# Kernel tuning notes

Measured on AMD Instinct MI355X. Metric: run time of the kernel, lower is better.

Reference implementation:

```python
import jax, jax.numpy as jnp
import numpy as np

HIDDEN = 100

def _lstm_step(h, c, gx, Whh, bhh):
    # gx: precomputed input contribution W_ih @ x + b_ih, shape [4H]
    gates = gx + Whh @ h + bhh
    i, f, g, o = jnp.split(gates, 4)
    i = jax.nn.sigmoid(i)
    f = jax.nn.sigmoid(f)
    g = jnp.tanh(g)
    o = jax.nn.sigmoid(o)
    c = f * c + i * g
    h = o * jnp.tanh(c)
    return h, c


def setup_inputs() -> dict:
    key = jax.random.key(0)
    ks = jax.random.split(key, 12)
    s = 0.1
    T_enc, T_dec = 4096, 4096
    return {
        "x": jax.random.normal(ks[0], (1, T_enc, 3), jnp.float32),
        "y": jax.random.randint(ks[1], (1, T_dec), 0, 6),
        "enc_Wih": jax.random.normal(ks[2], (4 * HIDDEN, 3), jnp.float32) * s,
        "enc_Whh": jax.random.normal(ks[3], (4 * HIDDEN, HIDDEN), jnp.float32) * s,
        "enc_bih": jax.random.normal(ks[4], (4 * HIDDEN,), jnp.float32) * s,
        "enc_bhh": jax.random.normal(ks[5], (4 * HIDDEN,), jnp.float32) * s,
        "dec_Wih": jax.random.normal(ks[6], (4 * HIDDEN, 1), jnp.float32) * s,
        "dec_Whh": jax.random.normal(ks[7], (4 * HIDDEN, HIDDEN), jnp.float32) * s,
        "dec_bih": jax.random.normal(ks[8], (4 * HIDDEN,), jnp.float32) * s,
        "dec_bhh": jax.random.normal(ks[9], (4 * HIDDEN,), jnp.float32) * s,
        "lin_W": jax.random.normal(ks[10], (6, HIDDEN), jnp.float32) * s,
        "lin_b": jax.random.normal(ks[11], (6,), jnp.float32) * s,
        "teacher_forcing_ratio": 1,
        "n_classes": 6,
    }


def reference(x, y, enc_Wih, enc_Whh, enc_bih, enc_bhh,
              dec_Wih, dec_Whh, dec_bih, dec_bhh, lin_W, lin_b,
              teacher_forcing_ratio, n_classes):
    T_dec = y.shape[1]
    # ---- Encoder: batch=1 LSTM over source sequence ----
    gx_enc = x[0] @ enc_Wih.T + enc_bih  # [T_enc, 4H]

    def enc_step(carry, gx):
        h, c = carry
        h, c = _lstm_step(h, c, gx, enc_Whh, enc_bhh)
        return (h, c), None

    h0 = jnp.zeros((HIDDEN,), x.dtype)
    (h_enc, c_enc), _ = jax.lax.scan(enc_step, (h0, h0), gx_enc)

    # ---- Decoder: single-step loop with teacher forcing ----
    yf = y[0].astype(jnp.float32)          # target labels fed as floats
    ratio = jnp.float32(teacher_forcing_ratio)
    u = jax.random.uniform(jax.random.key(1), (T_dec - 1,), jnp.float32)

    def dec_step(carry, inp):
        h, c, dec_in = carry
        u_t, y_t = inp
        gx = dec_in * dec_Wih[:, 0] + dec_bih  # scalar input -> [4H]
        h, c = _lstm_step(h, c, gx, dec_Whh, dec_bhh)
        logits = lin_W @ h + lin_b             # [n_classes]
        top_pred = jnp.argmax(logits).astype(jnp.float32)
        new_in = jnp.where(u_t < ratio, y_t, top_pred)
        return (h, c, new_in), logits

    _, logits_seq = jax.lax.scan(dec_step, (h_enc, c_enc, yf[0]), (u, yf[1:]))
    # outputs[0][t-1] = logits at step t, t = 1..T_dec-1; last row stays zero
    outputs = jnp.zeros((1, T_dec, n_classes), jnp.float32)
    outputs = outputs.at[0, : T_dec - 1].set(logits_seq)
    return outputs
```

## Files before the change

### kernel.cpp

```cpp
#include <hip/hip_runtime.h>

typedef _Float16 h2_t __attribute__((ext_vector_type(2)));

#define HID  100
#define TENC 4096
#define TDEC 4096
#define NCLS 6
#define NTHR 256

__device__ __forceinline__ float sigm(float v)  { return __builtin_amdgcn_rcpf(1.0f + __expf(-v)); }
__device__ __forceinline__ float tanh_(float v) { return 1.0f - 2.0f * __builtin_amdgcn_rcpf(1.0f + __expf(2.0f * v)); }

#define SYNC_LDS() asm volatile("s_waitcnt lgkmcnt(0)\n\ts_barrier" ::: "memory")

__device__ __forceinline__ float packh2(float a, float b) {
    h2_t p; p[0] = (_Float16)a; p[1] = (_Float16)b;
    return __builtin_bit_cast(float, p);
}

__device__ __forceinline__ float xsum1(float v) {
    const int s = __builtin_amdgcn_update_dpp(
        0, __builtin_bit_cast(int, v), 0xB1, 0xF, 0xF, true);
    return v + __builtin_bit_cast(float, s);
}

__device__ __forceinline__ float fd2(float w, float h, float acc) {
    return __builtin_amdgcn_fdot2(__builtin_bit_cast(h2_t, w),
                                  __builtin_bit_cast(h2_t, h), acc, false);
}

__global__ __launch_bounds__(NTHR, 1)
void lstm_rec(const float* __restrict__ x,
              const int*   __restrict__ y,
              const float* __restrict__ eWih,
              const float* __restrict__ eWhh,
              const float* __restrict__ ebih,
              const float* __restrict__ ebhh,
              const float* __restrict__ dWih,
              const float* __restrict__ dWhh,
              const float* __restrict__ dbih,
              const float* __restrict__ dbhh,
              float* __restrict__ hsto)
{
    __shared__ __align__(16) _Float16 hbuf[2][2][80];
    __shared__ __align__(8)  uint2    xst[TENC];
    __shared__               unsigned yst[TDEC];

    const int  t     = threadIdx.x;
    const int  w     = t >> 6;
    const int  l     = t & 63;
    const int  khalf = l & 1;
    const int  cell  = w * 32 + (l >> 1);
    const bool live  = (cell < HID);
    const int  k0    = khalf * 50;

    for (int i = t; i < TENC; i += NTHR) {
        const float a = x[3*i], b = x[3*i+1], cc = x[3*i+2];
        uint2 u;
        u.x = __builtin_bit_cast(unsigned, packh2(a, b));
        u.y = __builtin_bit_cast(unsigned, packh2(cc, 1.0f));
        xst[i] = u;
    }
    for (int i = t; i < TDEC; i += NTHR)
        yst[i] = __builtin_bit_cast(unsigned, packh2((float)y[i], 0.0f));
    for (int i = t; i < 2*2*80; i += NTHR) ((_Float16*)hbuf)[i] = (_Float16)0.0f;

    float wf[4][25];
    float wxp[4][2], bs[4];
    float c = 0.0f;
    #pragma unroll
    for (int r = 0; r < 4; ++r) {
        #pragma unroll
        for (int j = 0; j < 25; ++j) wf[r][j] = 0.0f;
        wxp[r][0] = wxp[r][1] = 0.0f; bs[r] = 0.0f;
    }
    if (live) {
        #pragma unroll
        for (int r = 0; r < 4; ++r) {
            const int row = cell + r * HID;
            #pragma unroll
            for (int j = 0; j < 25; ++j)
                wf[r][j] = packh2(eWhh[row*HID + k0 + 2*j], eWhh[row*HID + k0 + 2*j + 1]);
            if (khalf == 0) {
                wxp[r][0] = packh2(eWih[row*3+0], eWih[row*3+1]);
                wxp[r][1] = packh2(eWih[row*3+2], 0.0f);
                bs[r]     = ebih[row] + ebhh[row];
            }
        }
    }
    __syncthreads();

    const int hh2  = (cell < 50) ? 0 : 1;
    const int hoff = cell - 50 * hh2;

    int p = 0;

    for (int s = 0; s < TENC; ++s) {
        const float4* h4 = (const float4*)&hbuf[p][khalf][0];
        float hp[25];
        #pragma unroll
        for (int j = 0; j < 6; ++j) {
            const float4 v = h4[j];
            hp[4*j+0] = v.x; hp[4*j+1] = v.y; hp[4*j+2] = v.z; hp[4*j+3] = v.w;
        }
        hp[24] = ((const float*)h4)[24];

        const uint2 xp = xst[s];
        const float x0 = __builtin_bit_cast(float, xp.x);
        const float x1 = __builtin_bit_cast(float, xp.y);
        float a0 = fd2(wxp[0][0], x0, fd2(wxp[0][1], x1, bs[0]));
        float a1 = fd2(wxp[1][0], x0, fd2(wxp[1][1], x1, bs[1]));
        float a2 = fd2(wxp[2][0], x0, fd2(wxp[2][1], x1, bs[2]));
        float a3 = fd2(wxp[3][0], x0, fd2(wxp[3][1], x1, bs[3]));
        float b0 = 0.0f, b1 = 0.0f, b2 = 0.0f, b3 = 0.0f;
        #pragma unroll
        for (int j = 0; j < 12; ++j) {
            a0 = fd2(wf[0][j], hp[j], a0);
            a1 = fd2(wf[1][j], hp[j], a1);
            a2 = fd2(wf[2][j], hp[j], a2);
            a3 = fd2(wf[3][j], hp[j], a3);
        }
        #pragma unroll
        for (int j = 12; j < 25; ++j) {
            b0 = fd2(wf[0][j], hp[j], b0);
            b1 = fd2(wf[1][j], hp[j], b1);
            b2 = fd2(wf[2][j], hp[j], b2);
            b3 = fd2(wf[3][j], hp[j], b3);
        }
        a0 += b0; a1 += b1; a2 += b2; a3 += b3;

        a0 = xsum1(a0);
        a1 = xsum1(a1);
        a2 = xsum1(a2);
        a3 = xsum1(a3);

        const float fi = sigm(a0), ff = sigm(a1), fg = tanh_(a2), fo = sigm(a3);
        c = ff * c + fi * fg;
        const float hn = fo * tanh_(c);
        if (khalf == 0 && live)
            hbuf[p ^ 1][hh2][hoff] = (_Float16)hn;
        SYNC_LDS();
        p ^= 1;
    }

    float wdp[4], bsd[4];
    #pragma unroll
    for (int r = 0; r < 4; ++r) { wdp[r] = 0.0f; bsd[r] = 0.0f; }
    if (live) {
        #pragma unroll
        for (int r = 0; r < 4; ++r) {
            const int row = cell + r * HID;
            #pragma unroll
            for (int j = 0; j < 25; ++j)
                wf[r][j] = packh2(dWhh[row*HID + k0 + 2*j], dWhh[row*HID + k0 + 2*j + 1]);
            if (khalf == 0) {
                wdp[r] = packh2(dWih[row], 0.0f);
                bsd[r] = dbih[row] + dbhh[row];
            }
        }
    }

    for (int s = 0; s < TDEC - 1; ++s) {
        const float4* h4 = (const float4*)&hbuf[p][khalf][0];
        float hp[25];
        #pragma unroll
        for (int j = 0; j < 6; ++j) {
            const float4 v = h4[j];
            hp[4*j+0] = v.x; hp[4*j+1] = v.y; hp[4*j+2] = v.z; hp[4*j+3] = v.w;
        }
        hp[24] = ((const float*)h4)[24];

        const float yp = __builtin_bit_cast(float, yst[s]);
        float a0 = fd2(wdp[0], yp, bsd[0]);
        float a1 = fd2(wdp[1], yp, bsd[1]);
        float a2 = fd2(wdp[2], yp, bsd[2]);
        float a3 = fd2(wdp[3], yp, bsd[3]);
        float b0 = 0.0f, b1 = 0.0f, b2 = 0.0f, b3 = 0.0f;
        #pragma unroll
        for (int j = 0; j < 12; ++j) {
            a0 = fd2(wf[0][j], hp[j], a0);
            a1 = fd2(wf[1][j], hp[j], a1);
            a2 = fd2(wf[2][j], hp[j], a2);
            a3 = fd2(wf[3][j], hp[j], a3);
        }
        #pragma unroll
        for (int j = 12; j < 25; ++j) {
            b0 = fd2(wf[0][j], hp[j], b0);
            b1 = fd2(wf[1][j], hp[j], b1);
            b2 = fd2(wf[2][j], hp[j], b2);
            b3 = fd2(wf[3][j], hp[j], b3);
        }
        a0 += b0; a1 += b1; a2 += b2; a3 += b3;

        a0 = xsum1(a0);
        a1 = xsum1(a1);
        a2 = xsum1(a2);
        a3 = xsum1(a3);

        const float fi = sigm(a0), ff = sigm(a1), fg = tanh_(a2), fo = sigm(a3);
        c = ff * c + fi * fg;
        const float hn = fo * tanh_(c);
        if (live) {
            if (khalf == 0) {
                hbuf[p ^ 1][hh2][hoff] = (_Float16)hn;
            } else {
                hsto[s * HID + cell] = hn;
            }
        }
        SYNC_LDS();
        p ^= 1;
    }
}

__global__ __launch_bounds__(256)
void logits_k(const float* __restrict__ hsto, const float* __restrict__ linW,
              const float* __restrict__ linb, float* __restrict__ out)
{
    const int idx = blockIdx.x * 256 + threadIdx.x;
    if (idx >= TDEC * NCLS) return;
    const int tt = idx / NCLS;
    const int r  = idx % NCLS;
    if (tt >= TDEC - 1) { out[idx] = 0.0f; return; }
    const float* h  = hsto + tt * HID;
    const float* wr = linW + r * HID;
    float a = linb[r];
    #pragma unroll 4
    for (int k = 0; k < HID; ++k) a += wr[k] * h[k];
    out[idx] = a;
}

extern "C" void kernel_launch(void* const* d_in, const int* in_sizes, int n_in,
                              void* d_out, int out_size, void* d_ws, size_t ws_size,
                              hipStream_t stream)
{
    const float* x    = (const float*)d_in[0];
    const int*   y    = (const int*)  d_in[1];
    const float* eWih = (const float*)d_in[2];
    const float* eWhh = (const float*)d_in[3];
    const float* ebih = (const float*)d_in[4];
    const float* ebhh = (const float*)d_in[5];
    const float* dWih = (const float*)d_in[6];
    const float* dWhh = (const float*)d_in[7];
    const float* dbih = (const float*)d_in[8];
    const float* dbhh = (const float*)d_in[9];
    const float* linW = (const float*)d_in[10];
    const float* linb = (const float*)d_in[11];
    float* out  = (float*)d_out;
    float* hsto = (float*)d_ws;

    lstm_rec<<<dim3(1), dim3(NTHR), 0, stream>>>(
        x, y, eWih, eWhh, ebih, ebhh, dWih, dWhh, dbih, dbhh, hsto);

    const int nout = TDEC * NCLS;
    logits_k<<<dim3((nout + 255) / 256), dim3(256), 0, stream>>>(hsto, linW, linb, out);
}
```

Before: 3.589 ms.

## Fold input and bias into recurrent dot product and split gate activations across lane pair

Folds the input projection and bias into the recurrent fp16 dot-product by appending x (or y) and a constant 1 to the shared hidden buffer. The K split becomes 52/52 with 26 packed weight pairs per gate, which removes the separate input fdot2 chain. Each lane of a pair now computes two of the four gate nonlinearities and swaps them with DPP, halving transcendental work per lane. The single accumulator chain per gate is longer than the earlier two-chain split, which may add dependency latency.

```diff
diff --git a/kernel.cpp b/kernel.cpp
--- a/kernel.cpp
+++ b/kernel.cpp
@@ -18,18 +18,18 @@
     return __builtin_bit_cast(float, p);
 }
 
-__device__ __forceinline__ float xsum1(float v) {
-    const int s = __builtin_amdgcn_update_dpp(
-        0, __builtin_bit_cast(int, v), 0xB1, 0xF, 0xF, true);
-    return v + __builtin_bit_cast(float, s);
-}
-
 __device__ __forceinline__ float fd2(float w, float h, float acc) {
     return __builtin_amdgcn_fdot2(__builtin_bit_cast(h2_t, w),
                                   __builtin_bit_cast(h2_t, h), acc, false);
 }
 
-__global__ __launch_bounds__(NTHR, 1)
+__device__ __forceinline__ float dppB1(float v) {
+    return __builtin_bit_cast(float, __builtin_amdgcn_update_dpp(
+        0, __builtin_bit_cast(int, v), 0xB1, 0xF, 0xF, true));
+}
+__device__ __forceinline__ float xsum1(float v) { return v + dppB1(v); }
+
+__global__ __launch_bounds__(NTHR, 1) __attribute__((amdgpu_waves_per_eu(1, 1)))
 void lstm_rec(const float* __restrict__ x,
               const int*   __restrict__ y,
               const float* __restrict__ eWih,
@@ -42,7 +42,7 @@
               const float* __restrict__ dbhh,
               float* __restrict__ hsto)
 {
-    __shared__ __align__(16) _Float16 hbuf[2][2][80];
+    __shared__ __align__(16) _Float16 hbuf2[2][2][56];
     __shared__ __align__(8)  uint2    xst[TENC];
     __shared__               unsigned yst[TDEC];
 
@@ -52,7 +52,10 @@
     const int  khalf = l & 1;
     const int  cell  = w * 32 + (l >> 1);
     const bool live  = (cell < HID);
-    const int  k0    = khalf * 50;
+
+    const float cs = (khalf == 0) ?  2.0f : -1.0f;
+    const float ms = (khalf == 0) ? -2.0f :  1.0f;
+    const float as = (khalf == 0) ?  1.0f :  0.0f;
 
     for (int i = t; i < TENC; i += NTHR) {
         const float a = x[3*i], b = x[3*i+1], cc = x[3*i+2];
@@ -63,146 +66,181 @@
     }
     for (int i = t; i < TDEC; i += NTHR)
         yst[i] = __builtin_bit_cast(unsigned, packh2((float)y[i], 0.0f));
-    for (int i = t; i < 2*2*80; i += NTHR) ((_Float16*)hbuf)[i] = (_Float16)0.0f;
-
-    float wf[4][25];
-    float wxp[4][2], bs[4];
-    float c = 0.0f;
+    if (t < 2*2*56) ((_Float16*)hbuf2)[t] = (_Float16)0.0f;
+    __syncthreads();
+
+    if (t == 0) {
+        uint2 u;
+        u.x = __builtin_bit_cast(unsigned, packh2(x[0], x[1]));
+        u.y = __builtin_bit_cast(unsigned, packh2(x[2], 1.0f));
+        *(uint2*)&hbuf2[0][1][48] = u;
+    }
+
+    float wf[4][26];
     #pragma unroll
     for (int r = 0; r < 4; ++r) {
-        #pragma unroll
-        for (int j = 0; j < 25; ++j) wf[r][j] = 0.0f;
-        wxp[r][0] = wxp[r][1] = 0.0f; bs[r] = 0.0f;
-    }
-    if (live) {
-        #pragma unroll
-        for (int r = 0; r < 4; ++r) {
-            const int row = cell + r * HID;
-            #pragma unroll
-            for (int j = 0; j < 25; ++j)
-                wf[r][j] = packh2(eWhh[row*HID + k0 + 2*j], eWhh[row*HID + k0 + 2*j + 1]);
-            if (khalf == 0) {
-                wxp[r][0] = packh2(eWih[row*3+0], eWih[row*3+1]);
-                wxp[r][1] = packh2(eWih[row*3+2], 0.0f);
-                bs[r]     = ebih[row] + ebhh[row];
+        const int row = r*HID + cell;
+        #pragma unroll
+        for (int j = 0; j < 26; ++j) {
+            const int k0 = 52*khalf + 2*j, k1 = k0 + 1;
+            float v0 = 0.0f, v1 = 0.0f;
+            if (live) {
+                v0 = (k0 < HID) ? eWhh[row*HID + k0]
+                   : (k0 < 103) ? eWih[row*3 + (k0 - 100)] : (ebih[row] + ebhh[row]);
+                v1 = (k1 < HID) ? eWhh[row*HID + k1]
+                   : (k1 < 103) ? eWih[row*3 + (k1 - 100)] : (ebih[row] + ebhh[row]);
             }
-        }
-    }
-    __syncthreads();
-
-    const int hh2  = (cell < 50) ? 0 : 1;
-    const int hoff = cell - 50 * hh2;
-
+            wf[r][j] = packh2(v0, v1);
+        }
+    }
+    SYNC_LDS();
+
+    const int hh2  = (cell < 52) ? 0 : 1;
+    const int hoff = cell - 52*hh2;
+
+    float c = 0.0f;
     int p = 0;
 
     for (int s = 0; s < TENC; ++s) {
-        const float4* h4 = (const float4*)&hbuf[p][khalf][0];
-        float hp[25];
-        #pragma unroll
-        for (int j = 0; j < 6; ++j) {
-            const float4 v = h4[j];
-            hp[4*j+0] = v.x; hp[4*j+1] = v.y; hp[4*j+2] = v.z; hp[4*j+3] = v.w;
-        }
-        hp[24] = ((const float*)h4)[24];
-
-        const uint2 xp = xst[s];
-        const float x0 = __builtin_bit_cast(float, xp.x);
-        const float x1 = __builtin_bit_cast(float, xp.y);
-        float a0 = fd2(wxp[0][0], x0, fd2(wxp[0][1], x1, bs[0]));
-        float a1 = fd2(wxp[1][0], x0, fd2(wxp[1][1], x1, bs[1]));
-        float a2 = fd2(wxp[2][0], x0, fd2(wxp[2][1], x1, bs[2]));
-        float a3 = fd2(wxp[3][0], x0, fd2(wxp[3][1], x1, bs[3]));
-        float b0 = 0.0f, b1 = 0.0f, b2 = 0.0f, b3 = 0.0f;
-        #pragma unroll
-        for (int j = 0; j < 12; ++j) {
+        const _Float16* hr = &hbuf2[p][khalf][0];
+        float hp[26];
+        {
+            const float4 g0 = *(const float4*)&hr[0];
+            const float4 g1 = *(const float4*)&hr[8];
+            const float4 g2 = *(const float4*)&hr[16];
+            const float4 g3 = *(const float4*)&hr[24];
+            const float4 g4 = *(const float4*)&hr[32];
+            const float4 g5 = *(const float4*)&hr[40];
+            const float2 g6 = *(const float2*)&hr[48];
+            hp[0]=g0.x; hp[1]=g0.y; hp[2]=g0.z; hp[3]=g0.w;
+            hp[4]=g1.x; hp[5]=g1.y; hp[6]=g1.z; hp[7]=g1.w;
+            hp[8]=g2.x; hp[9]=g2.y; hp[10]=g2.z; hp[11]=g2.w;
+            hp[12]=g3.x; hp[13]=g3.y; hp[14]=g3.z; hp[15]=g3.w;
+            hp[16]=g4.x; hp[17]=g4.y; hp[18]=g4.z; hp[19]=g4.w;
+            hp[20]=g5.x; hp[21]=g5.y; hp[22]=g5.z; hp[23]=g5.w;
+            hp[24]=g6.x; hp[25]=g6.y;
+        }
+
+        if (t == 0 && s + 1 < TENC)
+            *(uint2*)&hbuf2[p ^ 1][1][48] = xst[s + 1];
+
+        float a0 = 0.0f, a1 = 0.0f, a2 = 0.0f, a3 = 0.0f;
+        #pragma unroll
+        for (int j = 0; j < 26; ++j) {
             a0 = fd2(wf[0][j], hp[j], a0);
             a1 = fd2(wf[1][j], hp[j], a1);
             a2 = fd2(wf[2][j], hp[j], a2);
             a3 = fd2(wf[3][j], hp[j], a3);
         }
-        #pragma unroll
-        for (int j = 12; j < 25; ++j) {
-            b0 = fd2(wf[0][j], hp[j], b0);
-            b1 = fd2(wf[1][j], hp[j], b1);
-            b2 = fd2(wf[2][j], hp[j], b2);
-            b3 = fd2(wf[3][j], hp[j], b3);
-        }
-        a0 += b0; a1 += b1; a2 += b2; a3 += b3;
-
         a0 = xsum1(a0);
         a1 = xsum1(a1);
         a2 = xsum1(a2);
         a3 = xsum1(a3);
 
-        const float fi = sigm(a0), ff = sigm(a1), fg = tanh_(a2), fo = sigm(a3);
-        c = ff * c + fi * fg;
+        const float uA = khalf ? a1 : a0;
+        const float rA = sigm(uA);
+        const float uB = khalf ? a3 : a2;
+        const float eB = __expf(uB * cs);
+        const float rB = __builtin_fmaf(__builtin_amdgcn_rcpf(1.0f + eB), ms, as);
+        const float sA = dppB1(rA);
+        const float sB = dppB1(rB);
+        const float fi = khalf ? sA : rA;
+        const float ff = khalf ? rA : sA;
+        const float fg = khalf ? sB : rB;
+        const float fo = khalf ? rB : sB;
+
+        c = __builtin_fmaf(ff, c, fi * fg);
         const float hn = fo * tanh_(c);
         if (khalf == 0 && live)
-            hbuf[p ^ 1][hh2][hoff] = (_Float16)hn;
+            hbuf2[p ^ 1][hh2][hoff] = (_Float16)hn;
         SYNC_LDS();
         p ^= 1;
     }
 
-    float wdp[4], bsd[4];
+    if (t == 0) {
+        uint2 v;
+        v.x = (yst[0] & 0xFFFFu) | 0x3C000000u;
+        v.y = 0u;
+        *(uint2*)&hbuf2[p][1][48] = v;
+    }
+
     #pragma unroll
-    for (int r = 0; r < 4; ++r) { wdp[r] = 0.0f; bsd[r] = 0.0f; }
-    if (live) {
-        #pragma unroll
-        for (int r = 0; r < 4; ++r) {
-            const int row = cell + r * HID;
-            #pragma unroll
-            for (int j = 0; j < 25; ++j)
-                wf[r][j] = packh2(dWhh[row*HID + k0 + 2*j], dWhh[row*HID + k0 + 2*j + 1]);
-            if (khalf == 0) {
-                wdp[r] = packh2(dWih[row], 0.0f);
-                bsd[r] = dbih[row] + dbhh[row];
+    for (int r = 0; r < 4; ++r) {
+        const int row = r*HID + cell;
+        #pragma unroll
+        for (int j = 0; j < 26; ++j) {
+            const int k0 = 52*khalf + 2*j, k1 = k0 + 1;
+            float v0 = 0.0f, v1 = 0.0f;
+            if (live) {
+                v0 = (k0 < HID) ? dWhh[row*HID + k0]
+                   : (k0 == 100) ? dWih[row]
+                   : (k0 == 101) ? (dbih[row] + dbhh[row]) : 0.0f;
+                v1 = (k1 < HID) ? dWhh[row*HID + k1]
+                   : (k1 == 100) ? dWih[row]
+                   : (k1 == 101) ? (dbih[row] + dbhh[row]) : 0.0f;
             }
-        }
-    }
+            wf[r][j] = packh2(v0, v1);
+        }
+    }
+    SYNC_LDS();
 
     for (int s = 0; s < TDEC - 1; ++s) {
-        const float4* h4 = (const float4*)&hbuf[p][khalf][0];
-        float hp[25];
-        #pragma unroll
-        for (int j = 0; j < 6; ++j) {
-            const float4 v = h4[j];
-            hp[4*j+0] = v.x; hp[4*j+1] = v.y; hp[4*j+2] = v.z; hp[4*j+3] = v.w;
-        }
-        hp[24] = ((const float*)h4)[24];
-
-        const float yp = __builtin_bit_cast(float, yst[s]);
-        float a0 = fd2(wdp[0], yp, bsd[0]);
-        float a1 = fd2(wdp[1], yp, bsd[1]);
-        float a2 = fd2(wdp[2], yp, bsd[2]);
-        float a3 = fd2(wdp[3], yp, bsd[3]);
-        float b0 = 0.0f, b1 = 0.0f, b2 = 0.0f, b3 = 0.0f;
-        #pragma unroll
-        for (int j = 0; j < 12; ++j) {
+        const _Float16* hr = &hbuf2[p][khalf][0];
+        float hp[26];
+        {
+            const float4 g0 = *(const float4*)&hr[0];
+            const float4 g1 = *(const float4*)&hr[8];
+            const float4 g2 = *(const float4*)&hr[16];
+            const float4 g3 = *(const float4*)&hr[24];
+            const float4 g4 = *(const float4*)&hr[32];
+            const float4 g5 = *(const float4*)&hr[40];
+            const float2 g6 = *(const float2*)&hr[48];
+            hp[0]=g0.x; hp[1]=g0.y; hp[2]=g0.z; hp[3]=g0.w;
+            hp[4]=g1.x; hp[5]=g1.y; hp[6]=g1.z; hp[7]=g1.w;
+            hp[8]=g2.x; hp[9]=g2.y; hp[10]=g2.z; hp[11]=g2.w;
+            hp[12]=g3.x; hp[13]=g3.y; hp[14]=g3.z; hp[15]=g3.w;
+            hp[16]=g4.x; hp[17]=g4.y; hp[18]=g4.z; hp[19]=g4.w;
+            hp[20]=g5.x; hp[21]=g5.y; hp[22]=g5.z; hp[23]=g5.w;
+            hp[24]=g6.x; hp[25]=g6.y;
+        }
+
+        if (t == 0 && s + 1 < TDEC - 1) {
+            uint2 v;
+            v.x = (yst[s + 1] & 0xFFFFu) | 0x3C000000u;
+            v.y = 0u;
+            *(uint2*)&hbuf2[p ^ 1][1][48] = v;
+        }
+
+        float a0 = 0.0f, a1 = 0.0f, a2 = 0.0f, a3 = 0.0f;
+        #pragma unroll
+        for (int j = 0; j < 26; ++j) {
             a0 = fd2(wf[0][j], hp[j], a0);
             a1 = fd2(wf[1][j], hp[j], a1);
             a2 = fd2(wf[2][j], hp[j], a2);
             a3 = fd2(wf[3][j], hp[j], a3);
         }
-        #pragma unroll
-        for (int j = 12; j < 25; ++j) {
-            b0 = fd2(wf[0][j], hp[j], b0);
-            b1 = fd2(wf[1][j], hp[j], b1);
-            b2 = fd2(wf[2][j], hp[j], b2);
-            b3 = fd2(wf[3][j], hp[j], b3);
-        }
-        a0 += b0; a1 += b1; a2 += b2; a3 += b3;
-
         a0 = xsum1(a0);
         a1 = xsum1(a1);
         a2 = xsum1(a2);
         a3 = xsum1(a3);
 
-        const float fi = sigm(a0), ff = sigm(a1), fg = tanh_(a2), fo = sigm(a3);
-        c = ff * c + fi * fg;
+        const float uA = khalf ? a1 : a0;
+        const float rA = sigm(uA);
+        const float uB = khalf ? a3 : a2;
+        const float eB = __expf(uB * cs);
+        const float rB = __builtin_fmaf(__builtin_amdgcn_rcpf(1.0f + eB), ms, as);
+        const float sA = dppB1(rA);
+        const float sB = dppB1(rB);
+        const float fi = khalf ? sA : rA;
+        const float ff = khalf ? rA : sA;
+        const float fg = khalf ? sB : rB;
+        const float fo = khalf ? rB : sB;
+
+        c = __builtin_fmaf(ff, c, fi * fg);
         const float hn = fo * tanh_(c);
         if (live) {
             if (khalf == 0) {
-                hbuf[p ^ 1][hh2][hoff] = (_Float16)hn;
+                hbuf2[p ^ 1][hh2][hoff] = (_Float16)hn;
             } else {
                 hsto[s * HID + cell] = hn;
             }
```

New measurement: 3.674 ms. +2.4%, slower.
